# Kernel optimization log

Hardware: AMD Instinct MI355X
Metric: run time of the kernel (lower is better)

## Reference

```python
import jax, jax.numpy as jnp
import numpy as np
from jax.ops import segment_sum, segment_max

DIM = 32   # hidden dim (hardcoded in Net)
N = 10000  # nodes
E = 160000 # edges
B = 64     # graphs in batch


def setup_inputs():
    key = jax.random.key(0)
    ks = jax.random.split(key, 16)
    r = lambda k, s: jax.random.normal(k, s, dtype=jnp.float32) * 0.1
    z = lambda s: jnp.zeros(s, jnp.float32)
    return {
        "x": jax.random.normal(ks[0], (N, 1), jnp.float32),
        "edge_attr": jax.random.normal(ks[1], (E, 2), jnp.float32),
        "lin0_w": r(ks[2], (1, DIM)), "lin0_b": z((DIM,)),
        "nn_w1": r(ks[3], (2, 128)), "nn_b1": z((128,)),
        "nn_w2": r(ks[4], (128, DIM * DIM)), "nn_b2": z((DIM * DIM,)),
        "conv_root": r(ks[5], (DIM, DIM)), "conv_bias": z((DIM,)),
        "gru_w_ih": r(ks[6], (DIM, 3 * DIM)), "gru_w_hh": r(ks[7], (DIM, 3 * DIM)),
        "gru_b_ih": z((3 * DIM,)), "gru_b_hh": z((3 * DIM,)),
        "lstm_w_ih": r(ks[8], (2 * DIM, 4 * DIM)), "lstm_w_hh": r(ks[9], (DIM, 4 * DIM)),
        "lstm_b_ih": z((4 * DIM,)), "lstm_b_hh": z((4 * DIM,)),
        "lin1_w": r(ks[10], (2 * DIM, DIM)), "lin1_b": z((DIM,)),
        "lin2_w": r(ks[11], (DIM, 1)), "lin2_b": z((1,)),
        "edge_index": jax.random.randint(ks[12], (2, E), 0, N),
        "batch": jnp.sort(jax.random.randint(ks[13], (N,), 0, B)),
    }


def _forward(x, edge_attr, params, edge_index, batch):
    (lin0_w, lin0_b, nn_w1, nn_b1, nn_w2, nn_b2, conv_root, conv_bias,
     gru_w_ih, gru_w_hh, gru_b_ih, gru_b_hh,
     lstm_w_ih, lstm_w_hh, lstm_b_ih, lstm_b_hh,
     lin1_w, lin1_b, lin2_w, lin2_b) = params
    src, dst = edge_index[0], edge_index[1]
    deg = jnp.maximum(segment_sum(jnp.ones((E,), x.dtype), dst, num_segments=N), 1.0)[:, None]
    # edge-conditioned weight matrices (depend only on edge_attr -> compute once)
    ew = (jax.nn.relu(edge_attr @ nn_w1 + nn_b1) @ nn_w2 + nn_b2).reshape(E, DIM, DIM)

    out = jax.nn.relu(x @ lin0_w + lin0_b)  # (N, DIM)
    h = out                                  # GRU hidden state
    for _ in range(3):
        # NNConv: gather -> per-edge matmul -> scatter-mean, plus root weight + bias
        msg = jnp.einsum('ei,eio->eo', out[src], ew)          # (E, DIM)
        agg = segment_sum(msg, dst, num_segments=N) / deg      # (N, DIM)
        m = jax.nn.relu(agg + out @ conv_root + conv_bias)
        # single GRU step (seq_len = 1)
        gi = m @ gru_w_ih + gru_b_ih
        gh = h @ gru_w_hh + gru_b_hh
        i_r, i_z, i_n = jnp.split(gi, 3, axis=-1)
        h_r, h_z, h_n = jnp.split(gh, 3, axis=-1)
        rg = jax.nn.sigmoid(i_r + h_r)
        zg = jax.nn.sigmoid(i_z + h_z)
        ng = jnp.tanh(i_n + rg * h_n)
        h = (1.0 - zg) * ng + zg * h
        out = h

    # Set2Set pooling, 3 processing steps
    q_star = jnp.zeros((B, 2 * DIM), x.dtype)
    hh = jnp.zeros((B, DIM), x.dtype)
    cc = jnp.zeros((B, DIM), x.dtype)
    for _ in range(3):
        gates = q_star @ lstm_w_ih + lstm_b_ih + hh @ lstm_w_hh + lstm_b_hh
        ig, fg, gg, og = jnp.split(gates, 4, axis=-1)  # torch gate order i,f,g,o
        cc = jax.nn.sigmoid(fg) * cc + jax.nn.sigmoid(ig) * jnp.tanh(gg)
        hh = jax.nn.sigmoid(og) * jnp.tanh(cc)
        q = hh                                          # (B, DIM)
        e = jnp.sum(out * q[batch], axis=-1)            # (N,)
        a = jnp.exp(e - segment_max(e, batch, num_segments=B)[batch])
        a = a / segment_sum(a, batch, num_segments=B)[batch]
        rvec = segment_sum(a[:, None] * out, batch, num_segments=B)  # (B, DIM)
        q_star = jnp.concatenate([q, rvec], axis=-1)

    y = jax.nn.relu(q_star @ lin1_w + lin1_b)
    return (y @ lin2_w + lin2_b).reshape(-1)  # (B,)


def reference(x, edge_attr, lin0_w, lin0_b, nn_w1, nn_b1, nn_w2, nn_b2, conv_root, conv_bias, gru_w_ih, gru_w_hh, gru_b_ih, gru_b_hh, lstm_w_ih, lstm_w_hh, lstm_b_ih, lstm_b_hh, lin1_w, lin1_b, lin2_w, lin2_b, edge_index, batch):
    params = (lin0_w, lin0_b, nn_w1, nn_b1, nn_w2, nn_b2, conv_root, conv_bias,
              gru_w_ih, gru_w_hh, gru_b_ih, gru_b_hh,
              lstm_w_ih, lstm_w_hh, lstm_b_ih, lstm_b_hh,
              lin1_w, lin1_b, lin2_w, lin2_b)
    return _forward(x, edge_attr, params, edge_index, batch)
```

## Files before the change

### kernel.cpp

```cpp
#include <hip/hip_runtime.h>
#include <math.h>

#define NN 10000
#define NE 160000
#define NG 64
#define DIM 32

typedef __attribute__((ext_vector_type(8))) short bf16x8;
typedef __attribute__((ext_vector_type(4))) float f32x4;

__device__ __forceinline__ float sigmoidf_(float x) { return 1.f / (1.f + expf(-x)); }

__device__ __forceinline__ unsigned short f2bf(float x) {
    unsigned u = __float_as_uint(x);
    u += 0x7FFF + ((u >> 16) & 1);
    return (unsigned short)(u >> 16);
}
__device__ __forceinline__ float bf2f(unsigned short b) {
    return __uint_as_float(((unsigned)b) << 16);
}

__global__ void k_setup(const float* __restrict__ w2, unsigned short* __restrict__ w2f,
                        const int* __restrict__ ei, int* __restrict__ cnt,
                        const float* __restrict__ x, const float* __restrict__ lw,
                        const float* __restrict__ lb, float* __restrict__ out,
                        const int* __restrict__ batch, int* __restrict__ gstart) {
    int b = blockIdx.x, t = threadIdx.x;
    if (b < 512) {
        int tid = b * 256 + t;
        int j = tid & 7, lane = (tid >> 3) & 63, tile = (tid >> 9) & 1;
        int s = (tid >> 10) & 3, i = tid >> 12;
        int h = s * 32 + ((lane >> 4) << 3) + j;
        int n = tile * 16 + (lane & 15);
        float v = w2[h * 1024 + i * 32 + n];
        unsigned short hi = f2bf(v);
        unsigned short lo = f2bf(v - bf2f(hi));
        int c = (i * 4 + s) * 2 + tile;
        w2f[(c * 2 + 0) * 512 + lane * 8 + j] = hi;
        w2f[(c * 2 + 1) * 512 + lane * 8 + j] = lo;
    } else if (b < 1137) {
        int e = (b - 512) * 256 + t;
        if (e < NE) atomicAdd(&cnt[ei[NE + e]], 1);
    } else if (b < 2387) {
        int idx = (b - 1137) * 256 + t;
        int n = idx >> 5, d = idx & 31;
        out[idx] = fmaxf(x[n] * lw[d] + lb[d], 0.f);
    } else {
        if (t <= NG) {
            int g = t, lo = 0, hi = NN;
            while (lo < hi) { int mid = (lo + hi) >> 1; if (batch[mid] < g) lo = mid + 1; else hi = mid; }
            gstart[g] = lo;
        }
    }
}

__global__ void k_scan(const int* __restrict__ cnt, int* __restrict__ row_start,
                       float* __restrict__ deg, int* __restrict__ perm) {
    __shared__ int sums[256];
    __shared__ int boff[64];
    int t = threadIdx.x;
    const int chunk = (NN + 255) / 256;
    int begin = t * chunk;
    int end = begin + chunk; if (end > NN) end = NN;
    int s = 0;
    for (int i = begin; i < end; ++i) s += cnt[i];
    sums[t] = s;
    __syncthreads();
    if (t == 0) {
        int acc = 0;
        for (int i = 0; i < 256; ++i) { int v = sums[i]; sums[i] = acc; acc += v; }
        row_start[NN] = acc;
    }
    __syncthreads();
    int acc = sums[t];
    for (int i = begin; i < end; ++i) {
        row_start[i] = acc;
        int c = cnt[i];
        deg[i] = (float)(c > 0 ? c : 1);
        acc += c;
    }
    if (t < 64) boff[t] = 0;
    __syncthreads();
    for (int i = begin; i < end; ++i)
        atomicAdd(&boff[min(cnt[i], 63)], 1);
    __syncthreads();
    if (t == 0) {
        int acc2 = 0;
        for (int b = 63; b >= 0; --b) { int v = boff[b]; boff[b] = acc2; acc2 += v; }
    }
    __syncthreads();
    for (int i = begin; i < end; ++i) {
        int b = min(cnt[i], 63);
        int p = atomicAdd(&boff[b], 1);
        perm[p] = i;
    }
}

__global__ void k_fill(const int* __restrict__ ei, const float* __restrict__ ea,
                       const int* __restrict__ row_start, int* __restrict__ cursor,
                       int* __restrict__ srt_src, float* __restrict__ srt_ea) {
    int e = blockIdx.x * 256 + threadIdx.x;
    if (e >= NE) return;
    int d = ei[NE + e];
    int p = atomicAdd(&cursor[d], 1);
    int pos = row_start[d] + p;
    srt_src[pos] = ei[e];
    srt_ea[2 * pos]     = ea[2 * e];
    srt_ea[2 * pos + 1] = ea[2 * e + 1];
}

#define NS 1040
#define PS 8320
__global__ __launch_bounds__(512, 4) void k_conv_gru(
    const int* __restrict__ row_start, const int* __restrict__ srt_src,
    const float* __restrict__ srt_ea, const int* __restrict__ perm,
    const float* __restrict__ w1, const float* __restrict__ b1,
    const unsigned short* __restrict__ w2f, const float* __restrict__ b2,
    const float* __restrict__ out_old, const float* __restrict__ deg,
    float* __restrict__ Sg,
    const float* __restrict__ root, const float* __restrict__ cbias,
    const float* __restrict__ wih, const float* __restrict__ whh,
    const float* __restrict__ bih, const float* __restrict__ bhh,
    float* __restrict__ out_new)
{
    __shared__ __align__(16) unsigned short RB[2 * PS];
    int t = threadIdx.x;
    int wave = t >> 6, lane = t & 63;
    int n0 = blockIdx.x * 8;
    int n = perm[n0 + wave];

    float Racc[64];
    #pragma unroll
    for (int i = 0; i < 64; ++i) Racc[i] = 0.f;
    float sacc = 0.f;

    float w1a0 = w1[lane],      w1c0 = w1[128 + lane],  bb0 = b1[lane];
    float w1a1 = w1[64 + lane], w1c1 = w1[192 + lane],  bb1 = b1[64 + lane];

    int rs = row_start[n], re = row_start[n + 1];
    const float2* eap = (const float2*)srt_ea;

    int p = rs;
    for (; p + 1 < re; p += 2) {
        int s0 = __builtin_amdgcn_readfirstlane(srt_src[p]);
        int s1 = __builtin_amdgcn_readfirstlane(srt_src[p + 1]);
        float2 a0 = eap[p];
        float2 a1 = eap[p + 1];
        const float* o0 = out_old + s0 * DIM;
        const float* o1 = out_old + s1 * DIM;
        float r00 = fmaxf(a0.x * w1a0 + a0.y * w1c0 + bb0, 0.f);
        float r01 = fmaxf(a0.x * w1a1 + a0.y * w1c1 + bb1, 0.f);
        float r10 = fmaxf(a1.x * w1a0 + a1.y * w1c0 + bb0, 0.f);
        float r11 = fmaxf(a1.x * w1a1 + a1.y * w1c1 + bb1, 0.f);
        #pragma unroll
        for (int q = 0; q < 32; ++q) {
            float v0 = o0[q];
            Racc[q]      += r00 * v0;
            Racc[32 + q] += r01 * v0;
        }
        #pragma unroll
        for (int q = 0; q < 32; ++q) {
            float v1 = o1[q];
            Racc[q]      += r10 * v1;
            Racc[32 + q] += r11 * v1;
        }
        if (lane < DIM) sacc += o0[lane] + o1[lane];
    }
    if (p < re) {
        int s0 = __builtin_amdgcn_readfirstlane(srt_src[p]);
        float2 a0 = eap[p];
        const float* o0 = out_old + s0 * DIM;
        float r00 = fmaxf(a0.x * w1a0 + a0.y * w1c0 + bb0, 0.f);
        float r01 = fmaxf(a0.x * w1a1 + a0.y * w1c1 + bb1, 0.f);
        #pragma unroll
        for (int q = 0; q < 32; ++q) {
            float v0 = o0[q];
            Racc[q]      += r00 * v0;
            Racc[32 + q] += r01 * v0;
        }
        if (lane < DIM) sacc += o0[lane];
    }
    if (lane < DIM) Sg[n * DIM + lane] = sacc;

    int quad = lane >> 4;
    int mm = lane & 7;
    unsigned aoff = (unsigned)(mm * NS + wave * 128 + quad * 8);
    f32x4 acc0 = {0.f, 0.f, 0.f, 0.f};
    f32x4 acc1 = {0.f, 0.f, 0.f, 0.f};

    unsigned short* Hw = RB + wave * NS;
    unsigned short* Lw = RB + PS + wave * NS;

    #pragma unroll
    for (int pass = 0; pass < 4; ++pass) {
        if (pass) __syncthreads();
        #pragma unroll
        for (int li = 0; li < 8; ++li) {
            float v0 = Racc[pass * 8 + li];
            float v1 = Racc[32 + pass * 8 + li];
            unsigned short h0 = f2bf(v0);
            unsigned short l0 = f2bf(v0 - bf2f(h0));
            unsigned short h1 = f2bf(v1);
            unsigned short l1 = f2bf(v1 - bf2f(h1));
            Hw[li * 128 + lane] = h0;  Hw[li * 128 + 64 + lane] = h1;
            Lw[li * 128 + lane] = l0;  Lw[li * 128 + 64 + lane] = l1;
        }
        __syncthreads();
        int ig = pass * 8 + wave;
        #pragma unroll
        for (int s = 0; s < 4; ++s) {
            bf16x8 ah = *(const bf16x8*)(RB + aoff + s * 32);
            bf16x8 al = *(const bf16x8*)(RB + PS + aoff + s * 32);
            const unsigned short* bp = w2f + (unsigned)((ig * 4 + s) * 2048 + lane * 8);
            bf16x8 bh0 = *(const bf16x8*)(bp);
            bf16x8 bl0 = *(const bf16x8*)(bp + 512);
            bf16x8 bh1 = *(const bf16x8*)(bp + 1024);
            bf16x8 bl1 = *(const bf16x8*)(bp + 1536);
            acc0 = __builtin_amdgcn_mfma_f32_16x16x32_bf16(ah, bh0, acc0, 0, 0, 0);
            acc0 = __builtin_amdgcn_mfma_f32_16x16x32_bf16(ah, bl0, acc0, 0, 0, 0);
            acc0 = __builtin_amdgcn_mfma_f32_16x16x32_bf16(al, bh0, acc0, 0, 0, 0);
            acc1 = __builtin_amdgcn_mfma_f32_16x16x32_bf16(ah, bh1, acc1, 0, 0, 0);
            acc1 = __builtin_amdgcn_mfma_f32_16x16x32_bf16(ah, bl1, acc1, 0, 0, 0);
            acc1 = __builtin_amdgcn_mfma_f32_16x16x32_bf16(al, bh1, acc1, 0, 0, 0);
        }
    }
    __syncthreads();

    float* part = (float*)RB;
    #pragma unroll
    for (int r = 0; r < 4; ++r) {
        part[((wave * 2 + 0) * 64 + lane) * 4 + r] = acc0[r];
        part[((wave * 2 + 1) * 64 + lane) * 4 + r] = acc1[r];
    }
    __syncthreads();

    if (t < 256) {
        int nb = t >> 5, d = t & 31;
        int nn_ = perm[n0 + nb];
        int base = t & 32;
        int tile = d >> 4, col = d & 15;
        int lidx = (nb >> 2) * 16 + col, reg = nb & 3;
        float aggv = 0.f;
        #pragma unroll
        for (int wv = 0; wv < 8; ++wv)
            aggv += part[((wv * 2 + tile) * 64 + lidx) * 4 + reg];

        float bt = 0.f;
        #pragma unroll 8
        for (int i = 0; i < DIM; ++i) bt += Sg[nn_ * DIM + i] * b2[i * DIM + d];
        aggv = (aggv + bt) / deg[nn_];

        float x = out_old[nn_ * DIM + d];
        float rootsum = 0.f;
        #pragma unroll 8
        for (int k = 0; k < DIM; ++k)
            rootsum += __shfl(x, base + k) * root[k * DIM + d];
        float m = fmaxf(aggv + rootsum + cbias[d], 0.f);

        float gir = bih[d], giz = bih[DIM + d], gin = bih[2 * DIM + d];
        float ghr = bhh[d], ghz = bhh[DIM + d], ghn = bhh[2 * DIM + d];
        #pragma unroll 4
        for (int k = 0; k < DIM; ++k) {
            float mk = __shfl(m, base + k);
            float hk = __shfl(x, base + k);
            gir += mk * wih[k * 96 + d];
            giz += mk * wih[k * 96 + DIM + d];
            gin += mk * wih[k * 96 + 2 * DIM + d];
            ghr += hk * whh[k * 96 + d];
            ghz += hk * whh[k * 96 + DIM + d];
            ghn += hk * whh[k * 96 + 2 * DIM + d];
        }
        float rg = sigmoidf_(gir + ghr);
        float zg = sigmoidf_(giz + ghz);
        float ng = tanhf(gin + rg * ghn);
        out_new[nn_ * DIM + d] = (1.f - zg) * ng + zg * x;
    }
}

__global__ __launch_bounds__(256) void k_set2set(
    const float* __restrict__ out, const int* __restrict__ gstart,
    const float* __restrict__ wih, const float* __restrict__ whh,
    const float* __restrict__ bih, const float* __restrict__ bhh,
    const float* __restrict__ l1w, const float* __restrict__ l1b,
    const float* __restrict__ l2w, const float* __restrict__ l2b,
    float* __restrict__ ebuf, float* __restrict__ y)
{
    __shared__ float swih[64 * 128];
    __shared__ float swhh[32 * 128];
    __shared__ float sq[2 * DIM];
    __shared__ float shh[DIM], scc[DIM];
    __shared__ float sgates[4 * DIM];
    __shared__ float sacc[8][DIM];
    __shared__ float sredA[4], sredB[4];

    int g = blockIdx.x, t = threadIdx.x;
    {
        const float4* wv = (const float4*)wih;   float4* sv = (float4*)swih;
        for (int i = t; i < 2048; i += 256) sv[i] = wv[i];
        const float4* wv2 = (const float4*)whh;  float4* sv2 = (float4*)swhh;
        for (int i = t; i < 1024; i += 256) sv2[i] = wv2[i];
    }
    if (t < 2 * DIM) sq[t] = 0.f;
    if (t < DIM) { shh[t] = 0.f; scc[t] = 0.f; }
    int ns = gstart[g], ne = gstart[g + 1];
    __syncthreads();

    for (int step = 0; step < 3; ++step) {
        if (t < 128) {
            float acc = bih[t] + bhh[t];
            #pragma unroll 8
            for (int k = 0; k < 2 * DIM; ++k) acc += sq[k] * swih[k * 128 + t];
            #pragma unroll 8
            for (int k = 0; k < DIM; ++k)     acc += shh[k] * swhh[k * 128 + t];
            sgates[t] = acc;
        }
        __syncthreads();
        if (t < DIM) {
            float ig = sigmoidf_(sgates[t]);
            float fg = sigmoidf_(sgates[DIM + t]);
            float gg = tanhf(sgates[2 * DIM + t]);
            float og = sigmoidf_(sgates[3 * DIM + t]);
            float c_new = fg * scc[t] + ig * gg;
            float h_new = og * tanhf(c_new);
            scc[t] = c_new;
            shh[t] = h_new;
            sq[t] = h_new;
        }
        __syncthreads();

        float lmax = -3.0e38f;
        for (int n = ns + t; n < ne; n += 256) {
            const float4* orow = (const float4*)(out + n * DIM);
            float e = 0.f;
            #pragma unroll
            for (int q = 0; q < 8; ++q) {
                float4 o4 = orow[q];
                e += o4.x * shh[4 * q] + o4.y * shh[4 * q + 1]
                   + o4.z * shh[4 * q + 2] + o4.w * shh[4 * q + 3];
            }
            ebuf[n] = e;
            lmax = fmaxf(lmax, e);
        }
        #pragma unroll
        for (int s = 1; s < 64; s <<= 1) lmax = fmaxf(lmax, __shfl_xor(lmax, s));
        if ((t & 63) == 0) sredA[t >> 6] = lmax;
        __syncthreads();
        float M = fmaxf(fmaxf(sredA[0], sredA[1]), fmaxf(sredA[2], sredA[3]));

        float lsum = 0.f;
        for (int n = ns + t; n < ne; n += 256) {
            float v = expf(ebuf[n] - M);
            ebuf[n] = v;
            lsum += v;
        }
        #pragma unroll
        for (int s = 1; s < 64; s <<= 1) lsum += __shfl_xor(lsum, s);
        if ((t & 63) == 0) sredB[t >> 6] = lsum;
        __syncthreads();
        float S = sredB[0] + sredB[1] + sredB[2] + sredB[3];
        float inv = (S > 0.f) ? 1.f / S : 0.f;

        int stp = t >> 5, d = t & 31;
        float racc = 0.f;
        for (int n = ns + stp; n < ne; n += 8)
            racc += ebuf[n] * out[n * DIM + d];
        sacc[stp][d] = racc;
        __syncthreads();
        if (t < DIM) {
            float r = 0.f;
            #pragma unroll
            for (int s = 0; s < 8; ++s) r += sacc[s][t];
            sq[DIM + t] = r * inv;
        }
        __syncthreads();
    }

    if (t < DIM) {
        float h = l1b[t];
        #pragma unroll 8
        for (int k = 0; k < 2 * DIM; ++k) h += sq[k] * l1w[k * DIM + t];
        float v = fmaxf(h, 0.f) * l2w[t];
        #pragma unroll
        for (int s = 1; s < 32; s <<= 1) v += __shfl_xor(v, s);
        if (t == 0) y[g] = v + l2b[0];
    }
}

extern "C" void kernel_launch(void* const* d_in, const int* in_sizes, int n_in,
                              void* d_out, int out_size, void* d_ws, size_t ws_size,
                              hipStream_t stream) {
    const float* x         = (const float*)d_in[0];
    const float* edge_attr = (const float*)d_in[1];
    const float* lin0_w    = (const float*)d_in[2];
    const float* lin0_b    = (const float*)d_in[3];
    const float* nn_w1     = (const float*)d_in[4];
    const float* nn_b1     = (const float*)d_in[5];
    const float* nn_w2     = (const float*)d_in[6];
    const float* nn_b2     = (const float*)d_in[7];
    const float* conv_root = (const float*)d_in[8];
    const float* conv_bias = (const float*)d_in[9];
    const float* gru_w_ih  = (const float*)d_in[10];
    const float* gru_w_hh  = (const float*)d_in[11];
    const float* gru_b_ih  = (const float*)d_in[12];
    const float* gru_b_hh  = (const float*)d_in[13];
    const float* lstm_w_ih = (const float*)d_in[14];
    const float* lstm_w_hh = (const float*)d_in[15];
    const float* lstm_b_ih = (const float*)d_in[16];
    const float* lstm_b_hh = (const float*)d_in[17];
    const float* lin1_w    = (const float*)d_in[18];
    const float* lin1_b    = (const float*)d_in[19];
    const float* lin2_w    = (const float*)d_in[20];
    const float* lin2_b    = (const float*)d_in[21];
    const int*   edge_index= (const int*)d_in[22];
    const int*   batch     = (const int*)d_in[23];
    float* yout = (float*)d_out;

    char* p = (char*)d_ws;
    auto alloc = [&](size_t bytes) { char* r = p; p += (bytes + 255) & ~(size_t)255; return r; };

    int*   cnt    = (int*)  alloc(NN * sizeof(int));
    int*   cursor = (int*)  alloc(NN * sizeof(int));
    size_t zero_bytes = (size_t)(p - (char*)d_ws);
    int*   row_start = (int*)  alloc((NN + 1) * sizeof(int));
    int*   gstart    = (int*)  alloc((NG + 1) * sizeof(int));
    int*   perm      = (int*)  alloc(NN * sizeof(int));
    int*   srt_src   = (int*)  alloc(NE * sizeof(int));
    float* srt_ea    = (float*)alloc(2 * NE * sizeof(float));
    float* deg       = (float*)alloc(NN * sizeof(float));
    float* outA      = (float*)alloc(NN * DIM * sizeof(float));
    float* outB      = (float*)alloc(NN * DIM * sizeof(float));
    float* Sg        = (float*)alloc(NN * DIM * sizeof(float));
    unsigned short* w2f = (unsigned short*)alloc(262144 * sizeof(unsigned short));
    float* ebuf      = (float*)alloc(NN * sizeof(float));
    (void)ws_size; (void)n_in; (void)in_sizes; (void)out_size;

    hipMemsetAsync(d_ws, 0, zero_bytes, stream);

    k_setup<<<2388, 256, 0, stream>>>(nn_w2, w2f, edge_index, cnt,
                                      x, lin0_w, lin0_b, outA, batch, gstart);
    k_scan <<<1,    256, 0, stream>>>(cnt, row_start, deg, perm);
    k_fill <<<625,  256, 0, stream>>>(edge_index, edge_attr, row_start, cursor, srt_src, srt_ea);

    const float* cur = outA;
    float* nxt = outB;
    for (int it = 0; it < 3; ++it) {
        k_conv_gru<<<1250, 512, 0, stream>>>(row_start, srt_src, srt_ea, perm,
                                             nn_w1, nn_b1, w2f, nn_b2,
                                             cur, deg, Sg,
                                             conv_root, conv_bias,
                                             gru_w_ih, gru_w_hh, gru_b_ih, gru_b_hh,
                                             nxt);
        const float* tmp = nxt; nxt = (float*)cur; cur = tmp;
    }
    const float* outF = cur;

    k_set2set<<<NG, 256, 0, stream>>>(outF, gstart,
                                      lstm_w_ih, lstm_w_hh, lstm_b_ih, lstm_b_hh,
                                      lin1_w, lin1_b, lin2_w, lin2_b, ebuf, yout);
}
```

Baseline: 363.1 us.

## Drop degree-sorted node permutation and pack edge records into float4

```diff
diff --git a/kernel.cpp b/kernel.cpp
--- a/kernel.cpp
+++ b/kernel.cpp
@@ -28,13 +28,12 @@
     int b = blockIdx.x, t = threadIdx.x;
     if (b < 512) {
         int tid = b * 256 + t;
-        int j = tid & 7, lane = (tid >> 3) & 63, tile = (tid >> 9) & 1;
-        int s = (tid >> 10) & 3, i = tid >> 12;
-        int h = s * 32 + ((lane >> 4) << 3) + j;
-        int n = tile * 16 + (lane & 15);
-        float v = w2[h * 1024 + i * 32 + n];
+        int h = tid >> 10, rem = tid & 1023, i = rem >> 5, n = rem & 31;
+        float v = w2[tid];
         unsigned short hi = f2bf(v);
         unsigned short lo = f2bf(v - bf2f(hi));
+        int s = h >> 5, hm = h & 31, q = hm >> 3, j = hm & 7;
+        int tile = n >> 4, nn = n & 15, lane = q * 16 + nn;
         int c = (i * 4 + s) * 2 + tile;
         w2f[(c * 2 + 0) * 512 + lane * 8 + j] = hi;
         w2f[(c * 2 + 1) * 512 + lane * 8 + j] = lo;
@@ -55,9 +54,8 @@
 }
 
 __global__ void k_scan(const int* __restrict__ cnt, int* __restrict__ row_start,
-                       float* __restrict__ deg, int* __restrict__ perm) {
+                       float* __restrict__ deg) {
     __shared__ int sums[256];
-    __shared__ int boff[64];
     int t = threadIdx.x;
     const int chunk = (NN + 255) / 256;
     int begin = t * chunk;
@@ -79,41 +77,28 @@
         deg[i] = (float)(c > 0 ? c : 1);
         acc += c;
     }
-    if (t < 64) boff[t] = 0;
-    __syncthreads();
-    for (int i = begin; i < end; ++i)
-        atomicAdd(&boff[min(cnt[i], 63)], 1);
-    __syncthreads();
-    if (t == 0) {
-        int acc2 = 0;
-        for (int b = 63; b >= 0; --b) { int v = boff[b]; boff[b] = acc2; acc2 += v; }
-    }
-    __syncthreads();
-    for (int i = begin; i < end; ++i) {
-        int b = min(cnt[i], 63);
-        int p = atomicAdd(&boff[b], 1);
-        perm[p] = i;
-    }
 }
 
 __global__ void k_fill(const int* __restrict__ ei, const float* __restrict__ ea,
                        const int* __restrict__ row_start, int* __restrict__ cursor,
-                       int* __restrict__ srt_src, float* __restrict__ srt_ea) {
+                       float4* __restrict__ erec) {
     int e = blockIdx.x * 256 + threadIdx.x;
     if (e >= NE) return;
     int d = ei[NE + e];
     int p = atomicAdd(&cursor[d], 1);
     int pos = row_start[d] + p;
-    srt_src[pos] = ei[e];
-    srt_ea[2 * pos]     = ea[2 * e];
-    srt_ea[2 * pos + 1] = ea[2 * e + 1];
+    float4 r;
+    r.x = __int_as_float(ei[e]);
+    r.y = ea[2 * e];
+    r.z = ea[2 * e + 1];
+    r.w = 0.f;
+    erec[pos] = r;
 }
 
 #define NS 1040
 #define PS 8320
 __global__ __launch_bounds__(512, 4) void k_conv_gru(
-    const int* __restrict__ row_start, const int* __restrict__ srt_src,
-    const float* __restrict__ srt_ea, const int* __restrict__ perm,
+    const int* __restrict__ row_start, const float4* __restrict__ erec,
     const float* __restrict__ w1, const float* __restrict__ b1,
     const unsigned short* __restrict__ w2f, const float* __restrict__ b2,
     const float* __restrict__ out_old, const float* __restrict__ deg,
@@ -127,7 +112,7 @@
     int t = threadIdx.x;
     int wave = t >> 6, lane = t & 63;
     int n0 = blockIdx.x * 8;
-    int n = perm[n0 + wave];
+    int n = n0 + wave;
 
     float Racc[64];
     #pragma unroll
@@ -138,20 +123,19 @@
     float w1a1 = w1[64 + lane], w1c1 = w1[192 + lane],  bb1 = b1[64 + lane];
 
     int rs = row_start[n], re = row_start[n + 1];
-    const float2* eap = (const float2*)srt_ea;
 
     int p = rs;
     for (; p + 1 < re; p += 2) {
-        int s0 = __builtin_amdgcn_readfirstlane(srt_src[p]);
-        int s1 = __builtin_amdgcn_readfirstlane(srt_src[p + 1]);
-        float2 a0 = eap[p];
-        float2 a1 = eap[p + 1];
+        float4 e0 = erec[p];
+        float4 e1 = erec[p + 1];
+        int s0 = __builtin_amdgcn_readfirstlane(__float_as_int(e0.x));
+        int s1 = __builtin_amdgcn_readfirstlane(__float_as_int(e1.x));
         const float* o0 = out_old + s0 * DIM;
         const float* o1 = out_old + s1 * DIM;
-        float r00 = fmaxf(a0.x * w1a0 + a0.y * w1c0 + bb0, 0.f);
-        float r01 = fmaxf(a0.x * w1a1 + a0.y * w1c1 + bb1, 0.f);
-        float r10 = fmaxf(a1.x * w1a0 + a1.y * w1c0 + bb0, 0.f);
-        float r11 = fmaxf(a1.x * w1a1 + a1.y * w1c1 + bb1, 0.f);
+        float r00 = fmaxf(e0.y * w1a0 + e0.z * w1c0 + bb0, 0.f);
+        float r01 = fmaxf(e0.y * w1a1 + e0.z * w1c1 + bb1, 0.f);
+        float r10 = fmaxf(e1.y * w1a0 + e1.z * w1c0 + bb0, 0.f);
+        float r11 = fmaxf(e1.y * w1a1 + e1.z * w1c1 + bb1, 0.f);
         #pragma unroll
         for (int q = 0; q < 32; ++q) {
             float v0 = o0[q];
@@ -167,11 +151,11 @@
         if (lane < DIM) sacc += o0[lane] + o1[lane];
     }
     if (p < re) {
-        int s0 = __builtin_amdgcn_readfirstlane(srt_src[p]);
-        float2 a0 = eap[p];
+        float4 e0 = erec[p];
+        int s0 = __builtin_amdgcn_readfirstlane(__float_as_int(e0.x));
         const float* o0 = out_old + s0 * DIM;
-        float r00 = fmaxf(a0.x * w1a0 + a0.y * w1c0 + bb0, 0.f);
-        float r01 = fmaxf(a0.x * w1a1 + a0.y * w1c1 + bb1, 0.f);
+        float r00 = fmaxf(e0.y * w1a0 + e0.z * w1c0 + bb0, 0.f);
+        float r01 = fmaxf(e0.y * w1a1 + e0.z * w1c1 + bb1, 0.f);
         #pragma unroll
         for (int q = 0; q < 32; ++q) {
             float v0 = o0[q];
@@ -236,7 +220,7 @@
 
     if (t < 256) {
         int nb = t >> 5, d = t & 31;
-        int nn_ = perm[n0 + nb];
+        int nn_ = n0 + nb;
         int base = t & 32;
         int tile = d >> 4, col = d & 15;
         int lidx = (nb >> 2) * 16 + col, reg = nb & 3;
@@ -423,9 +407,7 @@
     size_t zero_bytes = (size_t)(p - (char*)d_ws);
     int*   row_start = (int*)  alloc((NN + 1) * sizeof(int));
     int*   gstart    = (int*)  alloc((NG + 1) * sizeof(int));
-    int*   perm      = (int*)  alloc(NN * sizeof(int));
-    int*   srt_src   = (int*)  alloc(NE * sizeof(int));
-    float* srt_ea    = (float*)alloc(2 * NE * sizeof(float));
+    float4* erec     = (float4*)alloc(NE * sizeof(float4));
     float* deg       = (float*)alloc(NN * sizeof(float));
     float* outA      = (float*)alloc(NN * DIM * sizeof(float));
     float* outB      = (float*)alloc(NN * DIM * sizeof(float));
@@ -438,13 +420,13 @@
 
     k_setup<<<2388, 256, 0, stream>>>(nn_w2, w2f, edge_index, cnt,
                                       x, lin0_w, lin0_b, outA, batch, gstart);
-    k_scan <<<1,    256, 0, stream>>>(cnt, row_start, deg, perm);
-    k_fill <<<625,  256, 0, stream>>>(edge_index, edge_attr, row_start, cursor, srt_src, srt_ea);
+    k_scan <<<1,    256, 0, stream>>>(cnt, row_start, deg);
+    k_fill <<<625,  256, 0, stream>>>(edge_index, edge_attr, row_start, cursor, erec);
 
     const float* cur = outA;
     float* nxt = outB;
     for (int it = 0; it < 3; ++it) {
-        k_conv_gru<<<1250, 512, 0, stream>>>(row_start, srt_src, srt_ea, perm,
+        k_conv_gru<<<1250, 512, 0, stream>>>(row_start, erec,
                                              nn_w1, nn_b1, w2f, nn_b2,
                                              cur, deg, Sg,
                                              conv_root, conv_bias,
```

Result: no change. 363.7 us (+0.2%).
